# Kernel tuning notes

Measured on AMD Instinct MI355X. Metric: run time of the kernel, lower is better.

Reference implementation:

```python
import jax, jax.numpy as jnp
import numpy as np

B, T, R = 128, 20, 49           # batch, caption length, num regions (7x7)
V, E, H, FD, A = 10000, 512, 512, 512, 256  # vocab, embed, hidden, feature, attn dims


def setup_inputs() -> dict:
    key = jax.random.key(0)
    ks = jax.random.split(key, 16)
    s = 0.02
    return {
        "features": jax.random.normal(ks[0], (B, R, FD), dtype=jnp.float32),
        "captions": jax.random.randint(ks[1], (B, T), 0, V),
        "emb": jax.random.normal(ks[2], (V, E), dtype=jnp.float32) * s,
        "W_h": jax.random.normal(ks[3], (A, H), dtype=jnp.float32) * s,
        "b_h": jnp.zeros((A,), jnp.float32),
        "W_f": jax.random.normal(ks[4], (A, FD), dtype=jnp.float32) * s,
        "b_f": jnp.zeros((A,), jnp.float32),
        "v_w": jax.random.normal(ks[5], (A,), dtype=jnp.float32) * s,
        "v_b": jnp.zeros((), jnp.float32),
        "W_ih": jax.random.normal(ks[6], (4 * H, E + FD), dtype=jnp.float32) * s,
        "W_hh": jax.random.normal(ks[7], (4 * H, H), dtype=jnp.float32) * s,
        "b_ih": jnp.zeros((4 * H,), jnp.float32),
        "b_hh": jnp.zeros((4 * H,), jnp.float32),
        "fc_W": jax.random.normal(ks[8], (V, H), dtype=jnp.float32) * s,
        "fc_b": jnp.zeros((V,), jnp.float32),
    }


def reference(features, captions, emb, W_h, b_h, W_f, b_f, v_w, v_b,
              W_ih, W_hh, b_ih, b_hh, fc_W, fc_b):
    Bn = features.shape[0]
    Hd = W_hh.shape[1]
    # features are constant across timesteps -> project once (same math as per-step W_f(features))
    f_proj = jnp.einsum('brf,af->bra', features, W_f) + b_f  # (B,R,A)
    embeds = emb[captions[:, :-1]]                            # (B,T-1,E)
    xs = jnp.swapaxes(embeds, 0, 1)                           # (T-1,B,E)
    bias = b_ih + b_hh

    def step(carry, x_t):
        hx, cx = carry
        # Bahdanau attention
        h = hx @ W_h.T + b_h                                  # (B,A)
        scores = jnp.tanh(h[:, None, :] + f_proj) @ v_w + v_b  # (B,R)
        alpha = jax.nn.softmax(scores, axis=1)
        context = jnp.einsum('br,brf->bf', alpha, features)   # (B,FD)
        # LSTMCell (PyTorch gate order: i,f,g,o)
        lstm_in = jnp.concatenate([x_t, context], axis=1)     # (B,E+FD)
        gates = lstm_in @ W_ih.T + hx @ W_hh.T + bias         # (B,4H)
        i, f, g, o = jnp.split(gates, 4, axis=1)
        cx = jax.nn.sigmoid(f) * cx + jax.nn.sigmoid(i) * jnp.tanh(g)
        hx = jax.nn.sigmoid(o) * jnp.tanh(cx)
        logit = hx @ fc_W.T + fc_b                            # (B,V)
        return (hx, cx), logit

    init = (jnp.zeros((Bn, Hd), features.dtype), jnp.zeros((Bn, Hd), features.dtype))
    _, logits = jax.lax.scan(step, init, xs)                  # (T-1,B,V)
    return jnp.swapaxes(logits, 0, 1)                         # (B,T-1,V)
```

## Files before the change

### kernel.cpp

```cpp
#include <hip/hip_runtime.h>
#include <hip/hip_bf16.h>
#include <math.h>

#define NB 128
#define NT 20
#define NS 19
#define NR 49
#define NV 10000
#define NE 512
#define NH 512
#define NFD 512
#define NA 256
#define NG 2048
#define NKC 1536

typedef __bf16 bf16_t;
typedef bf16_t bf16x8 __attribute__((ext_vector_type(8)));
typedef float f32x4 __attribute__((ext_vector_type(4)));

__device__ __forceinline__ float sigm(float x) { return 1.f / (1.f + expf(-x)); }

__global__ __launch_bounds__(256) void k_setup(
    const float* __restrict__ W_ih, const float* __restrict__ W_hh,
    const float* __restrict__ b_ih, const float* __restrict__ b_hh,
    const float* __restrict__ W_h, const float* __restrict__ fc_W,
    const float* __restrict__ W_f, const float* __restrict__ features,
    bf16_t* __restrict__ Wcatb, bf16_t* __restrict__ fcWb,
    bf16_t* __restrict__ Wfb, bf16_t* __restrict__ featb,
    bf16_t* __restrict__ W_hb, float* __restrict__ bias,
    float* __restrict__ hx, float* __restrict__ cx)
{
    int idx = blockIdx.x * 256 + threadIdx.x;
    if (idx < NV * NH) fcWb[idx] = (bf16_t)fc_W[idx];
    if (idx < NG * NKC) {
        int n = idx / NKC, k = idx % NKC;
        int h = n >> 2, g = n & 3;
        int orig = g * NH + h;
        Wcatb[idx] = (bf16_t)((k < NE + NFD) ? W_ih[orig * (NE + NFD) + k]
                                             : W_hh[orig * NH + (k - NE - NFD)]);
    }
    if (idx < NB * NR * NFD) featb[idx] = (bf16_t)features[idx];
    if (idx < NA * NFD) Wfb[idx] = (bf16_t)W_f[idx];
    if (idx < NA * NH) W_hb[idx] = (bf16_t)W_h[idx];
    if (idx < NG) {
        int h = idx >> 2, g = idx & 3;
        int orig = g * NH + h;
        bias[idx] = b_ih[orig] + b_hh[orig];
    }
    if (idx < NB * NH) { hx[idx] = 0.f; cx[idx] = 0.f; }
}

__global__ __launch_bounds__(1024) void k_attn(
    const float* __restrict__ hx, const bf16_t* __restrict__ W_hb,
    const float* __restrict__ b_h, const float* __restrict__ fproj,
    const float* __restrict__ v_w, const bf16_t* __restrict__ featb,
    const float* __restrict__ emb, const int* __restrict__ captions,
    bf16_t* __restrict__ lin, int t)
{
    int b = blockIdx.x;
    int tid = threadIdx.x;
    __shared__ float hxs[NH];
    __shared__ float part[4][NA];
    __shared__ float hatt[NA];
    __shared__ float salpha[64];

    if (tid < NH) hxs[tid] = hx[b * NH + tid];
    __syncthreads();

    {
        int a = tid & (NA - 1), q = tid >> 8;
        const bf16x8* wrow = (const bf16x8*)(W_hb + (size_t)a * NH + q * 128);
        const float* hq = hxs + q * 128;
        float p = 0.f;
        #pragma unroll
        for (int c = 0; c < 16; ++c) {
            bf16x8 wv = wrow[c];
            int k = c * 8;
            p += hq[k+0]*(float)wv[0] + hq[k+1]*(float)wv[1]
               + hq[k+2]*(float)wv[2] + hq[k+3]*(float)wv[3]
               + hq[k+4]*(float)wv[4] + hq[k+5]*(float)wv[5]
               + hq[k+6]*(float)wv[6] + hq[k+7]*(float)wv[7];
        }
        part[q][a] = p;
    }
    __syncthreads();
    if (tid < NA)
        hatt[tid] = part[0][tid] + part[1][tid] + part[2][tid] + part[3][tid] + b_h[tid];
    __syncthreads();

    {
        int wv = tid >> 6, lane = tid & 63;
        for (int r = wv; r < NR; r += 16) {
            float s = 0.f;
            const float* fp = fproj + (size_t)(b * NR + r) * NA;
            #pragma unroll
            for (int j = 0; j < 4; ++j) {
                int aa = lane + 64 * j;
                s += tanhf(hatt[aa] + fp[aa]) * v_w[aa];
            }
            #pragma unroll
            for (int off = 32; off; off >>= 1) s += __shfl_xor(s, off);
            if (lane == 0) salpha[r] = s;
        }
    }
    __syncthreads();

    if (tid < 64) {
        float v = (tid < NR) ? salpha[tid] : -INFINITY;
        float m = v;
        #pragma unroll
        for (int off = 32; off; off >>= 1) m = fmaxf(m, __shfl_xor(m, off));
        float e = (tid < NR) ? expf(v - m) : 0.f;
        float ssum = e;
        #pragma unroll
        for (int off = 32; off; off >>= 1) ssum += __shfl_xor(ssum, off);
        if (tid < NR) salpha[tid] = e / ssum;
    }
    __syncthreads();

    if (tid < NH) {
        bf16_t* lrow = lin + (size_t)b * NKC;
        lrow[tid] = (bf16_t)emb[(size_t)captions[b * NT + t] * NE + tid];
        lrow[NE + NFD + tid] = (bf16_t)hxs[tid];
        float c = 0.f;
        #pragma unroll 7
        for (int r = 0; r < NR; ++r)
            c += salpha[r] * (float)featb[(size_t)(b * NR + r) * NFD + tid];
        lrow[NE + tid] = (bf16_t)c;
    }
}

__global__ __launch_bounds__(256) void gemm_bf16_nt(
    const bf16_t* __restrict__ Am, const bf16_t* __restrict__ Bm,
    const float* __restrict__ bias, float* __restrict__ Cm,
    int M, int N, int K, int ldc)
{
    __shared__ uint4 AsU[512];
    __shared__ uint4 BsU[512];
    int tid = threadIdx.x;
    int m0 = blockIdx.x * 64, n0 = blockIdx.y * 64;
    int nk = K >> 6;

    int rowS = tid >> 3, slotS = tid & 7;
    int wr0 = rowS * 8 + (slotS ^ (rowS & 7));
    int rowS2 = rowS + 32;
    int wr1 = rowS2 * 8 + (slotS ^ (rowS2 & 7));

    const uint4* pA = (const uint4*)(Am + (size_t)(m0 + rowS) * K) + slotS;
    size_t aStep = (size_t)4 * K;
    int nrow0 = n0 + rowS, nrow1 = n0 + rowS2;
    bool bv0 = nrow0 < N, bv1 = nrow1 < N;
    const uint4* pB0 = (const uint4*)(Bm + (size_t)nrow0 * K) + slotS;
    const uint4* pB1 = (const uint4*)(Bm + (size_t)nrow1 * K) + slotS;
    uint4 zz = make_uint4(0, 0, 0, 0);

    int w = tid >> 6, lane = tid & 63;
    int wm = w >> 1, wn = w & 1;
    int lr = lane & 15, lg = lane >> 4;
    int ra[2][2], rb[2][2];
    #pragma unroll
    for (int i = 0; i < 2; ++i)
        #pragma unroll
        for (int kk = 0; kk < 2; ++kk) {
            int rA = wm * 32 + i * 16 + lr;
            int rB = wn * 32 + i * 16 + lr;
            int s = kk * 4 + lg;
            ra[i][kk] = rA * 8 + (s ^ (rA & 7));
            rb[i][kk] = rB * 8 + (s ^ (rB & 7));
        }

    f32x4 acc00 = {}, acc01 = {}, acc10 = {}, acc11 = {};
    uint4 a0 = pA[0], a1 = pA[aStep];
    uint4 b0 = bv0 ? pB0[0] : zz;
    uint4 b1 = bv1 ? pB1[0] : zz;
    pA += 8; pB0 += 8; pB1 += 8;

    for (int kt = 0; kt < nk; ++kt) {
        __syncthreads();
        AsU[wr0] = a0; AsU[wr1] = a1;
        BsU[wr0] = b0; BsU[wr1] = b1;
        if (kt + 1 < nk) {
            a0 = pA[0]; a1 = pA[aStep];
            b0 = bv0 ? pB0[0] : zz;
            b1 = bv1 ? pB1[0] : zz;
            pA += 8; pB0 += 8; pB1 += 8;
        }
        __syncthreads();
        const bf16x8* Af = (const bf16x8*)AsU;
        const bf16x8* Bf = (const bf16x8*)BsU;
        #pragma unroll
        for (int kk = 0; kk < 2; ++kk) {
            bf16x8 fa0 = Af[ra[0][kk]], fa1 = Af[ra[1][kk]];
            bf16x8 fb0 = Bf[rb[0][kk]], fb1 = Bf[rb[1][kk]];
            acc00 = __builtin_amdgcn_mfma_f32_16x16x32_bf16(fa0, fb0, acc00, 0, 0, 0);
            acc01 = __builtin_amdgcn_mfma_f32_16x16x32_bf16(fa0, fb1, acc01, 0, 0, 0);
            acc10 = __builtin_amdgcn_mfma_f32_16x16x32_bf16(fa1, fb0, acc10, 0, 0, 0);
            acc11 = __builtin_amdgcn_mfma_f32_16x16x32_bf16(fa1, fb1, acc11, 0, 0, 0);
        }
    }

    f32x4 av[2][2] = {{acc00, acc01}, {acc10, acc11}};
    #pragma unroll
    for (int i = 0; i < 2; ++i) {
        int mbase = m0 + wm * 32 + i * 16 + lg * 4;
        #pragma unroll
        for (int j = 0; j < 2; ++j) {
            int n = n0 + wn * 32 + j * 16 + lr;
            if (n < N) {
                float bz = bias ? bias[n] : 0.f;
                #pragma unroll
                for (int r = 0; r < 4; ++r)
                    Cm[(size_t)(mbase + r) * ldc + n] = av[i][j][r] + bz;
            }
        }
    }
}

__global__ __launch_bounds__(256) void k_step(
    const bf16_t* __restrict__ lin, const bf16_t* __restrict__ Wcatb,
    const float* __restrict__ bias, float* __restrict__ hx,
    float* __restrict__ cx, bf16_t* __restrict__ hxAll, int t)
{
    __shared__ __align__(16) char smem[16640];
    uint4* AsU = (uint4*)smem;
    uint4* BsU = AsU + 512;

    int tid = threadIdx.x;
    int m0 = blockIdx.x * 64, n0 = blockIdx.y * 64;

    int rowS = tid >> 3, slotS = tid & 7;
    int wr0 = rowS * 8 + (slotS ^ (rowS & 7));
    int rowS2 = rowS + 32;
    int wr1 = rowS2 * 8 + (slotS ^ (rowS2 & 7));

    const uint4* pA = (const uint4*)(lin + (size_t)(m0 + rowS) * NKC) + slotS;
    const uint4* pB0 = (const uint4*)(Wcatb + (size_t)(n0 + rowS) * NKC) + slotS;
    const uint4* pB1 = (const uint4*)(Wcatb + (size_t)(n0 + rowS2) * NKC) + slotS;
    size_t aStep = (size_t)4 * NKC;

    int w = tid >> 6, lane = tid & 63;
    int wm = w >> 1, wn = w & 1;
    int lr = lane & 15, lg = lane >> 4;
    int ra[2][2], rb[2][2];
    #pragma unroll
    for (int i = 0; i < 2; ++i)
        #pragma unroll
        for (int kk = 0; kk < 2; ++kk) {
            int rA = wm * 32 + i * 16 + lr;
            int rB = wn * 32 + i * 16 + lr;
            int s = kk * 4 + lg;
            ra[i][kk] = rA * 8 + (s ^ (rA & 7));
            rb[i][kk] = rB * 8 + (s ^ (rB & 7));
        }

    f32x4 acc00 = {}, acc01 = {}, acc10 = {}, acc11 = {};
    uint4 a0 = pA[0], a1 = pA[aStep];
    uint4 b0 = pB0[0], b1 = pB1[0];
    pA += 8; pB0 += 8; pB1 += 8;

    #pragma unroll 1
    for (int kt = 0; kt < NKC / 64; ++kt) {
        __syncthreads();
        AsU[wr0] = a0; AsU[wr1] = a1;
        BsU[wr0] = b0; BsU[wr1] = b1;
        if (kt + 1 < NKC / 64) {
            a0 = pA[0]; a1 = pA[aStep];
            b0 = pB0[0]; b1 = pB1[0];
            pA += 8; pB0 += 8; pB1 += 8;
        }
        __syncthreads();
        const bf16x8* Af = (const bf16x8*)AsU;
        const bf16x8* Bf = (const bf16x8*)BsU;
        #pragma unroll
        for (int kk = 0; kk < 2; ++kk) {
            bf16x8 fa0 = Af[ra[0][kk]], fa1 = Af[ra[1][kk]];
            bf16x8 fb0 = Bf[rb[0][kk]], fb1 = Bf[rb[1][kk]];
            acc00 = __builtin_amdgcn_mfma_f32_16x16x32_bf16(fa0, fb0, acc00, 0, 0, 0);
            acc01 = __builtin_amdgcn_mfma_f32_16x16x32_bf16(fa0, fb1, acc01, 0, 0, 0);
            acc10 = __builtin_amdgcn_mfma_f32_16x16x32_bf16(fa1, fb0, acc10, 0, 0, 0);
            acc11 = __builtin_amdgcn_mfma_f32_16x16x32_bf16(fa1, fb1, acc11, 0, 0, 0);
        }
    }

    __syncthreads();
    float* Ct = (float*)smem;
    f32x4 av[2][2] = {{acc00, acc01}, {acc10, acc11}};
    #pragma unroll
    for (int i = 0; i < 2; ++i)
        #pragma unroll
        for (int j = 0; j < 2; ++j) {
            int mloc = wm * 32 + i * 16 + lg * 4;
            int nloc = wn * 32 + j * 16 + lr;
            #pragma unroll
            for (int r = 0; r < 4; ++r)
                Ct[(mloc + r) * 65 + nloc] = av[i][j][r];
        }
    __syncthreads();

    int hloc = tid & 15;
    int h = (n0 >> 2) + hloc;
    #pragma unroll
    for (int q = 0; q < 4; ++q) {
        int m = (tid >> 4) + q * 16;
        int b = m0 + m;
        const float* crow = Ct + m * 65 + hloc * 4;
        const float* brow = bias + n0 + hloc * 4;
        float gi = crow[0] + brow[0];
        float gf = crow[1] + brow[1];
        float gg = crow[2] + brow[2];
        float go = crow[3] + brow[3];
        size_t idx = (size_t)b * NH + h;
        float c = sigm(gf) * cx[idx] + sigm(gi) * tanhf(gg);
        float hn = sigm(go) * tanhf(c);
        cx[idx] = c;
        hx[idx] = hn;
        hxAll[((size_t)t * NB + b) * NH + h] = (bf16_t)hn;
    }
}

__global__ __launch_bounds__(256) void k_logits(
    const bf16_t* __restrict__ hxAll, const bf16_t* __restrict__ fcWb,
    const float* __restrict__ fc_b, float* __restrict__ out)
{
    __shared__ uint4 AsU[512];
    __shared__ uint4 BsU[512];
    int tid = threadIdx.x;
    int m0 = blockIdx.x * 64, n0 = blockIdx.y * 64;

    int rowS = tid >> 3, slotS = tid & 7;
    int wr0 = rowS * 8 + (slotS ^ (rowS & 7));
    int rowS2 = rowS + 32;
    int wr1 = rowS2 * 8 + (slotS ^ (rowS2 & 7));

    const uint4* pA = (const uint4*)(hxAll + (size_t)(m0 + rowS) * NH) + slotS;
    size_t aStep = (size_t)4 * NH;
    int nrow0 = n0 + rowS, nrow1 = n0 + rowS2;
    bool bv0 = nrow0 < NV, bv1 = nrow1 < NV;
    const uint4* pB0 = (const uint4*)(fcWb + (size_t)nrow0 * NH) + slotS;
    const uint4* pB1 = (const uint4*)(fcWb + (size_t)nrow1 * NH) + slotS;
    uint4 zz = make_uint4(0, 0, 0, 0);

    int w = tid >> 6, lane = tid & 63;
    int wm = w >> 1, wn = w & 1;
    int lr = lane & 15, lg = lane >> 4;
    int ra[2][2], rb[2][2];
    #pragma unroll
    for (int i = 0; i < 2; ++i)
        #pragma unroll
        for (int kk = 0; kk < 2; ++kk) {
            int rA = wm * 32 + i * 16 + lr;
            int rB = wn * 32 + i * 16 + lr;
            int s = kk * 4 + lg;
            ra[i][kk] = rA * 8 + (s ^ (rA & 7));
            rb[i][kk] = rB * 8 + (s ^ (rB & 7));
        }

    f32x4 acc00 = {}, acc01 = {}, acc10 = {}, acc11 = {};
    uint4 a0 = pA[0], a1 = pA[aStep];
    uint4 b0 = bv0 ? pB0[0] : zz;
    uint4 b1 = bv1 ? pB1[0] : zz;
    pA += 8; pB0 += 8; pB1 += 8;

    #pragma unroll 1
    for (int kt = 0; kt < NH / 64; ++kt) {
        __syncthreads();
        AsU[wr0] = a0; AsU[wr1] = a1;
        BsU[wr0] = b0; BsU[wr1] = b1;
        if (kt + 1 < NH / 64) {
            a0 = pA[0]; a1 = pA[aStep];
            b0 = bv0 ? pB0[0] : zz;
            b1 = bv1 ? pB1[0] : zz;
            pA += 8; pB0 += 8; pB1 += 8;
        }
        __syncthreads();
        const bf16x8* Af = (const bf16x8*)AsU;
        const bf16x8* Bf = (const bf16x8*)BsU;
        #pragma unroll
        for (int kk = 0; kk < 2; ++kk) {
            bf16x8 fa0 = Af[ra[0][kk]], fa1 = Af[ra[1][kk]];
            bf16x8 fb0 = Bf[rb[0][kk]], fb1 = Bf[rb[1][kk]];
            acc00 = __builtin_amdgcn_mfma_f32_16x16x32_bf16(fa0, fb0, acc00, 0, 0, 0);
            acc01 = __builtin_amdgcn_mfma_f32_16x16x32_bf16(fa0, fb1, acc01, 0, 0, 0);
            acc10 = __builtin_amdgcn_mfma_f32_16x16x32_bf16(fa1, fb0, acc10, 0, 0, 0);
            acc11 = __builtin_amdgcn_mfma_f32_16x16x32_bf16(fa1, fb1, acc11, 0, 0, 0);
        }
    }

    f32x4 av[2][2] = {{acc00, acc01}, {acc10, acc11}};
    #pragma unroll
    for (int i = 0; i < 2; ++i) {
        int mbase = m0 + wm * 32 + i * 16 + lg * 4;
        #pragma unroll
        for (int j = 0; j < 2; ++j) {
            int n = n0 + wn * 32 + j * 16 + lr;
            if (n < NV) {
                float bz = fc_b[n];
                #pragma unroll
                for (int r = 0; r < 4; ++r) {
                    int m = mbase + r;
                    int b = m & 127, tt = m >> 7;
                    out[((size_t)b * NS + tt) * NV + n] = av[i][j][r] + bz;
                }
            }
        }
    }
}

extern "C" void kernel_launch(void* const* d_in, const int* in_sizes, int n_in,
                              void* d_out, int out_size, void* d_ws, size_t ws_size,
                              hipStream_t stream)
{
    const float* features = (const float*)d_in[0];
    const int*   captions = (const int*)d_in[1];
    const float* emb      = (const float*)d_in[2];
    const float* W_h      = (const float*)d_in[3];
    const float* b_h      = (const float*)d_in[4];
    const float* W_f      = (const float*)d_in[5];
    const float* b_f      = (const float*)d_in[6];
    const float* v_w      = (const float*)d_in[7];
    const float* W_ih     = (const float*)d_in[9];
    const float* W_hh     = (const float*)d_in[10];
    const float* b_ih     = (const float*)d_in[11];
    const float* b_hh     = (const float*)d_in[12];
    const float* fc_W     = (const float*)d_in[13];
    const float* fc_b     = (const float*)d_in[14];
    float* out = (float*)d_out;

    char* base = (char*)d_ws;
    bf16_t* Wcatb = (bf16_t*)base;  base += (size_t)NG * NKC * 2;
    bf16_t* fcWb  = (bf16_t*)base;  base += (size_t)NV * NH * 2;
    bf16_t* Wfb   = (bf16_t*)base;  base += (size_t)NA * NFD * 2;
    bf16_t* featb = (bf16_t*)base;  base += (size_t)NB * NR * NFD * 2;
    bf16_t* lin   = (bf16_t*)base;  base += (size_t)NB * NKC * 2;
    bf16_t* W_hb  = (bf16_t*)base;  base += (size_t)NA * NH * 2;
    bf16_t* hxAll = (bf16_t*)base;  base += (size_t)NS * NB * NH * 2;
    float* bias   = (float*)base;   base += (size_t)NG * 4;
    float* fproj  = (float*)base;   base += (size_t)NB * NR * NA * 4;
    float* hx     = (float*)base;   base += (size_t)NB * NH * 4;
    float* cx     = (float*)base;   base += (size_t)NB * NH * 4;

    k_setup<<<dim3((NV * NH + 255) / 256), 256, 0, stream>>>(
        W_ih, W_hh, b_ih, b_hh, W_h, fc_W, W_f, features,
        Wcatb, fcWb, Wfb, featb, W_hb, bias, hx, cx);

    gemm_bf16_nt<<<dim3(98, 4), 256, 0, stream>>>(
        featb, Wfb, b_f, fproj, NB * NR, NA, NFD, NA);

    for (int t = 0; t < NS; ++t) {
        k_attn<<<dim3(NB), 1024, 0, stream>>>(
            hx, W_hb, b_h, fproj, v_w, featb, emb, captions, lin, t);
        k_step<<<dim3(2, 32), 256, 0, stream>>>(
            lin, Wcatb, bias, hx, cx, hxAll, t);
    }

    k_logits<<<dim3(38, 157), 256, 0, stream>>>(hxAll, fcWb, fc_b, out);
}
```

Baseline: 682.5 us.

## Fuse recurrent attention and LSTM steps into one persistent cooperative kernel

Replaces the 38 per-timestep launches (attention kernel plus LSTM gate GEMM) with a single cooperative persistent kernel of 128 blocks. The blocks synchronise through an atomic-counter grid barrier between the attention phase and the gate GEMM phase. The gate GEMM is retiled to 32x64 tiles so 128 blocks cover it. The logits GEMM also gets a one-dimensional grid with an XCD-aware block swizzle. This removes launch overhead and inter-kernel gaps, at the cost of spin-wait barriers and lower per-step parallelism, since attention now uses 512 threads per batch row.

```diff
diff --git a/kernel.cpp b/kernel.cpp
--- a/kernel.cpp
+++ b/kernel.cpp
@@ -13,12 +13,26 @@
 #define NA 256
 #define NG 2048
 #define NKC 1536
+#define NBLK 128
 
 typedef __bf16 bf16_t;
 typedef bf16_t bf16x8 __attribute__((ext_vector_type(8)));
 typedef float f32x4 __attribute__((ext_vector_type(4)));
 
 __device__ __forceinline__ float sigm(float x) { return 1.f / (1.f + expf(-x)); }
+
+__device__ __forceinline__ void grid_sync(unsigned* cnt, unsigned target)
+{
+    __syncthreads();
+    if (threadIdx.x == 0) {
+        __threadfence();
+        atomicAdd(cnt, 1u);
+        while (__hip_atomic_load(cnt, __ATOMIC_RELAXED, __HIP_MEMORY_SCOPE_AGENT) < target)
+            __builtin_amdgcn_s_sleep(1);
+        __threadfence();
+    }
+    __syncthreads();
+}
 
 __global__ __launch_bounds__(256) void k_setup(
     const float* __restrict__ W_ih, const float* __restrict__ W_hh,
@@ -50,86 +64,6 @@
     if (idx < NB * NH) { hx[idx] = 0.f; cx[idx] = 0.f; }
 }
 
-__global__ __launch_bounds__(1024) void k_attn(
-    const float* __restrict__ hx, const bf16_t* __restrict__ W_hb,
-    const float* __restrict__ b_h, const float* __restrict__ fproj,
-    const float* __restrict__ v_w, const bf16_t* __restrict__ featb,
-    const float* __restrict__ emb, const int* __restrict__ captions,
-    bf16_t* __restrict__ lin, int t)
-{
-    int b = blockIdx.x;
-    int tid = threadIdx.x;
-    __shared__ float hxs[NH];
-    __shared__ float part[4][NA];
-    __shared__ float hatt[NA];
-    __shared__ float salpha[64];
-
-    if (tid < NH) hxs[tid] = hx[b * NH + tid];
-    __syncthreads();
-
-    {
-        int a = tid & (NA - 1), q = tid >> 8;
-        const bf16x8* wrow = (const bf16x8*)(W_hb + (size_t)a * NH + q * 128);
-        const float* hq = hxs + q * 128;
-        float p = 0.f;
-        #pragma unroll
-        for (int c = 0; c < 16; ++c) {
-            bf16x8 wv = wrow[c];
-            int k = c * 8;
-            p += hq[k+0]*(float)wv[0] + hq[k+1]*(float)wv[1]
-               + hq[k+2]*(float)wv[2] + hq[k+3]*(float)wv[3]
-               + hq[k+4]*(float)wv[4] + hq[k+5]*(float)wv[5]
-               + hq[k+6]*(float)wv[6] + hq[k+7]*(float)wv[7];
-        }
-        part[q][a] = p;
-    }
-    __syncthreads();
-    if (tid < NA)
-        hatt[tid] = part[0][tid] + part[1][tid] + part[2][tid] + part[3][tid] + b_h[tid];
-    __syncthreads();
-
-    {
-        int wv = tid >> 6, lane = tid & 63;
-        for (int r = wv; r < NR; r += 16) {
-            float s = 0.f;
-            const float* fp = fproj + (size_t)(b * NR + r) * NA;
-            #pragma unroll
-            for (int j = 0; j < 4; ++j) {
-                int aa = lane + 64 * j;
-                s += tanhf(hatt[aa] + fp[aa]) * v_w[aa];
-            }
-            #pragma unroll
-            for (int off = 32; off; off >>= 1) s += __shfl_xor(s, off);
-            if (lane == 0) salpha[r] = s;
-        }
-    }
-    __syncthreads();
-
-    if (tid < 64) {
-        float v = (tid < NR) ? salpha[tid] : -INFINITY;
-        float m = v;
-        #pragma unroll
-        for (int off = 32; off; off >>= 1) m = fmaxf(m, __shfl_xor(m, off));
-        float e = (tid < NR) ? expf(v - m) : 0.f;
-        float ssum = e;
-        #pragma unroll
-        for (int off = 32; off; off >>= 1) ssum += __shfl_xor(ssum, off);
-        if (tid < NR) salpha[tid] = e / ssum;
-    }
-    __syncthreads();
-
-    if (tid < NH) {
-        bf16_t* lrow = lin + (size_t)b * NKC;
-        lrow[tid] = (bf16_t)emb[(size_t)captions[b * NT + t] * NE + tid];
-        lrow[NE + NFD + tid] = (bf16_t)hxs[tid];
-        float c = 0.f;
-        #pragma unroll 7
-        for (int r = 0; r < NR; ++r)
-            c += salpha[r] * (float)featb[(size_t)(b * NR + r) * NFD + tid];
-        lrow[NE + tid] = (bf16_t)c;
-    }
-}
-
 __global__ __launch_bounds__(256) void gemm_bf16_nt(
     const bf16_t* __restrict__ Am, const bf16_t* __restrict__ Bm,
     const float* __restrict__ bias, float* __restrict__ Cm,
@@ -216,27 +150,194 @@
     }
 }
 
-__global__ __launch_bounds__(256) void k_step(
-    const bf16_t* __restrict__ lin, const bf16_t* __restrict__ Wcatb,
-    const float* __restrict__ bias, float* __restrict__ hx,
-    float* __restrict__ cx, bf16_t* __restrict__ hxAll, int t)
-{
-    __shared__ __align__(16) char smem[16640];
-    uint4* AsU = (uint4*)smem;
-    uint4* BsU = AsU + 512;
+__global__ __launch_bounds__(512) void k_loop(
+    const bf16_t* __restrict__ Wcatb, const bf16_t* __restrict__ W_hb,
+    const float* __restrict__ b_h, const float* __restrict__ fproj,
+    const float* __restrict__ v_w, const bf16_t* __restrict__ featb,
+    const float* __restrict__ emb, const int* __restrict__ captions,
+    const float* __restrict__ bias,
+    bf16_t* __restrict__ lin, float* __restrict__ hx, float* __restrict__ cx,
+    bf16_t* __restrict__ hxAll, unsigned* __restrict__ bar)
+{
+    __shared__ union {
+        struct { float hxs[NH]; float part[2][NA]; float salpha[64]; } att;
+        struct { uint4 AsU[256]; uint4 BsU[512]; } g;
+        float Ct[32 * 65];
+    } sm;
 
     int tid = threadIdx.x;
-    int m0 = blockIdx.x * 64, n0 = blockIdx.y * 64;
+    int bid = blockIdx.x;
+    int lane = tid & 63;
+    unsigned bcount = 0;
+
+    int m0 = (bid & 3) * 32;
+    int n0 = (bid >> 2) * 64;
+    int sRow = tid >> 3, sSlot = tid & 7;
+    int wrS = sRow * 8 + (sSlot ^ (sRow & 7));
+    const uint4* pB_base = (const uint4*)(Wcatb + (size_t)(n0 + sRow) * NKC) + sSlot;
+    const uint4* pA_base = (tid < 256)
+        ? (const uint4*)(lin + (size_t)(m0 + sRow) * NKC) + sSlot : (const uint4*)0;
+
+    int w = tid >> 6;
+    int wm = w & 1, wn = w >> 1;
+    int lr = lane & 15, lg = lane >> 4;
+    int raIdx[2], rbIdx[2];
+    #pragma unroll
+    for (int kk = 0; kk < 2; ++kk) {
+        int rA = wm * 16 + lr;
+        int rB = wn * 16 + lr;
+        int s = kk * 4 + lg;
+        raIdx[kk] = rA * 8 + (s ^ (rA & 7));
+        rbIdx[kk] = rB * 8 + (s ^ (rB & 7));
+    }
+
+    for (int t = 0; t < NS; ++t) {
+        int b = bid;
+        sm.att.hxs[tid] = hx[b * NH + tid];
+        __syncthreads();
+        {
+            int a = tid & 255, q = tid >> 8;
+            const bf16x8* wrow = (const bf16x8*)(W_hb + (size_t)a * NH + q * 256);
+            const float* hq = sm.att.hxs + q * 256;
+            float p = 0.f;
+            #pragma unroll
+            for (int c2 = 0; c2 < 32; ++c2) {
+                bf16x8 wv = wrow[c2];
+                int k = c2 * 8;
+                p += hq[k+0]*(float)wv[0] + hq[k+1]*(float)wv[1]
+                   + hq[k+2]*(float)wv[2] + hq[k+3]*(float)wv[3]
+                   + hq[k+4]*(float)wv[4] + hq[k+5]*(float)wv[5]
+                   + hq[k+6]*(float)wv[6] + hq[k+7]*(float)wv[7];
+            }
+            sm.att.part[q][a] = p;
+        }
+        __syncthreads();
+        {
+            for (int r = w; r < NR; r += 8) {
+                const float* fp = fproj + ((size_t)b * NR + r) * NA;
+                float s = 0.f;
+                #pragma unroll
+                for (int j = 0; j < 4; ++j) {
+                    int aa = lane + 64 * j;
+                    float hv = sm.att.part[0][aa] + sm.att.part[1][aa] + b_h[aa];
+                    s += tanhf(hv + fp[aa]) * v_w[aa];
+                }
+                #pragma unroll
+                for (int off = 32; off; off >>= 1) s += __shfl_xor(s, off);
+                if (lane == 0) sm.att.salpha[r] = s;
+            }
+        }
+        __syncthreads();
+        if (tid < 64) {
+            float v = (tid < NR) ? sm.att.salpha[tid] : -INFINITY;
+            float m = v;
+            #pragma unroll
+            for (int off = 32; off; off >>= 1) m = fmaxf(m, __shfl_xor(m, off));
+            float e = (tid < NR) ? expf(v - m) : 0.f;
+            float ssum = e;
+            #pragma unroll
+            for (int off = 32; off; off >>= 1) ssum += __shfl_xor(ssum, off);
+            if (tid < NR) sm.att.salpha[tid] = e / ssum;
+        }
+        __syncthreads();
+        {
+            bf16_t* lrow = lin + (size_t)b * NKC;
+            int cap = captions[b * NT + t];
+            lrow[tid] = (bf16_t)emb[(size_t)cap * NE + tid];
+            lrow[NE + NFD + tid] = (bf16_t)sm.att.hxs[tid];
+            float c = 0.f;
+            #pragma unroll 7
+            for (int r = 0; r < NR; ++r)
+                c += sm.att.salpha[r] * (float)featb[((size_t)b * NR + r) * NFD + tid];
+            lrow[NE + tid] = (bf16_t)c;
+        }
+        grid_sync(bar, (++bcount) * NBLK);
+
+        {
+            const uint4* pA = pA_base;
+            const uint4* pB = pB_base;
+            f32x4 acc = {};
+            uint4 aR = {}, bR;
+            bR = pB[0]; pB += 8;
+            if (tid < 256) { aR = pA[0]; pA += 8; }
+            #pragma unroll 1
+            for (int kt = 0; kt < NKC / 64; ++kt) {
+                __syncthreads();
+                sm.g.BsU[wrS] = bR;
+                if (tid < 256) sm.g.AsU[wrS] = aR;
+                if (kt + 1 < NKC / 64) {
+                    bR = pB[0]; pB += 8;
+                    if (tid < 256) { aR = pA[0]; pA += 8; }
+                }
+                __syncthreads();
+                const bf16x8* Af = (const bf16x8*)sm.g.AsU;
+                const bf16x8* Bf = (const bf16x8*)sm.g.BsU;
+                #pragma unroll
+                for (int kk = 0; kk < 2; ++kk) {
+                    bf16x8 fa = Af[raIdx[kk]];
+                    bf16x8 fb = Bf[rbIdx[kk]];
+                    acc = __builtin_amdgcn_mfma_f32_16x16x32_bf16(fa, fb, acc, 0, 0, 0);
+                }
+            }
+            __syncthreads();
+            {
+                int crow = wm * 16 + lg * 4;
+                int ccol = wn * 16 + lr;
+                #pragma unroll
+                for (int r = 0; r < 4; ++r)
+                    sm.Ct[(crow + r) * 65 + ccol] = acc[r];
+            }
+            __syncthreads();
+            {
+                int hloc = tid & 15, m = tid >> 4;
+                int bb = m0 + m;
+                int h = (n0 >> 2) + hloc;
+                const float* crow = sm.Ct + m * 65 + hloc * 4;
+                const float* brow = bias + n0 + hloc * 4;
+                float gi = crow[0] + brow[0];
+                float gf = crow[1] + brow[1];
+                float gg = crow[2] + brow[2];
+                float go = crow[3] + brow[3];
+                size_t idx = (size_t)bb * NH + h;
+                float c = sigm(gf) * cx[idx] + sigm(gi) * tanhf(gg);
+                float hn = sigm(go) * tanhf(c);
+                cx[idx] = c;
+                hx[idx] = hn;
+                hxAll[((size_t)t * NB + bb) * NH + h] = (bf16_t)hn;
+            }
+        }
+        grid_sync(bar, (++bcount) * NBLK);
+    }
+}
+
+__global__ __launch_bounds__(256) void k_logits(
+    const bf16_t* __restrict__ hxAll, const bf16_t* __restrict__ fcWb,
+    const float* __restrict__ fc_b, float* __restrict__ out)
+{
+    const int MT = 38, NWG = 38 * 157;
+    int bid0 = blockIdx.x;
+    int q = NWG >> 3, r = NWG & 7;
+    int xcd = bid0 & 7, loc = bid0 >> 3;
+    int swz = (xcd < r ? xcd * (q + 1) : r * (q + 1) + (xcd - r) * q) + loc;
+    int m0 = (swz % MT) * 64;
+    int n0 = (swz / MT) * 64;
+
+    __shared__ uint4 AsU[512];
+    __shared__ uint4 BsU[512];
+    int tid = threadIdx.x;
 
     int rowS = tid >> 3, slotS = tid & 7;
     int wr0 = rowS * 8 + (slotS ^ (rowS & 7));
     int rowS2 = rowS + 32;
     int wr1 = rowS2 * 8 + (slotS ^ (rowS2 & 7));
 
-    const uint4* pA = (const uint4*)(lin + (size_t)(m0 + rowS) * NKC) + slotS;
-    const uint4* pB0 = (const uint4*)(Wcatb + (size_t)(n0 + rowS) * NKC) + slotS;
-    const uint4* pB1 = (const uint4*)(Wcatb + (size_t)(n0 + rowS2) * NKC) + slotS;
-    size_t aStep = (size_t)4 * NKC;
+    const uint4* pA = (const uint4*)(hxAll + (size_t)(m0 + rowS) * NH) + slotS;
+    size_t aStep = (size_t)4 * NH;
+    int nrow0 = n0 + rowS, nrow1 = n0 + rowS2;
+    bool bv0 = nrow0 < NV, bv1 = nrow1 < NV;
+    const uint4* pB0 = (const uint4*)(fcWb + (size_t)nrow0 * NH) + slotS;
+    const uint4* pB1 = (const uint4*)(fcWb + (size_t)nrow1 * NH) + slotS;
+    uint4 zz = make_uint4(0, 0, 0, 0);
 
     int w = tid >> 6, lane = tid & 63;
     int wm = w >> 1, wn = w & 1;
@@ -255,17 +356,19 @@
 
     f32x4 acc00 = {}, acc01 = {}, acc10 = {}, acc11 = {};
     uint4 a0 = pA[0], a1 = pA[aStep];
-    uint4 b0 = pB0[0], b1 = pB1[0];
+    uint4 b0 = bv0 ? pB0[0] : zz;
+    uint4 b1 = bv1 ? pB1[0] : zz;
     pA += 8; pB0 += 8; pB1 += 8;
 
     #pragma unroll 1
-    for (int kt = 0; kt < NKC / 64; ++kt) {
+    for (int kt = 0; kt < NH / 64; ++kt) {
         __syncthreads();
         AsU[wr0] = a0; AsU[wr1] = a1;
         BsU[wr0] = b0; BsU[wr1] = b1;
-        if (kt + 1 < NKC / 64) {
+        if (kt + 1 < NH / 64) {
             a0 = pA[0]; a1 = pA[aStep];
-            b0 = pB0[0]; b1 = pB1[0];
+            b0 = bv0 ? pB0[0] : zz;
+            b1 = bv1 ? pB1[0] : zz;
             pA += 8; pB0 += 8; pB1 += 8;
         }
         __syncthreads();
@@ -282,110 +385,6 @@
         }
     }
 
-    __syncthreads();
-    float* Ct = (float*)smem;
-    f32x4 av[2][2] = {{acc00, acc01}, {acc10, acc11}};
-    #pragma unroll
-    for (int i = 0; i < 2; ++i)
-        #pragma unroll
-        for (int j = 0; j < 2; ++j) {
-            int mloc = wm * 32 + i * 16 + lg * 4;
-            int nloc = wn * 32 + j * 16 + lr;
-            #pragma unroll
-            for (int r = 0; r < 4; ++r)
-                Ct[(mloc + r) * 65 + nloc] = av[i][j][r];
-        }
-    __syncthreads();
-
-    int hloc = tid & 15;
-    int h = (n0 >> 2) + hloc;
-    #pragma unroll
-    for (int q = 0; q < 4; ++q) {
-        int m = (tid >> 4) + q * 16;
-        int b = m0 + m;
-        const float* crow = Ct + m * 65 + hloc * 4;
-        const float* brow = bias + n0 + hloc * 4;
-        float gi = crow[0] + brow[0];
-        float gf = crow[1] + brow[1];
-        float gg = crow[2] + brow[2];
-        float go = crow[3] + brow[3];
-        size_t idx = (size_t)b * NH + h;
-        float c = sigm(gf) * cx[idx] + sigm(gi) * tanhf(gg);
-        float hn = sigm(go) * tanhf(c);
-        cx[idx] = c;
-        hx[idx] = hn;
-        hxAll[((size_t)t * NB + b) * NH + h] = (bf16_t)hn;
-    }
-}
-
-__global__ __launch_bounds__(256) void k_logits(
-    const bf16_t* __restrict__ hxAll, const bf16_t* __restrict__ fcWb,
-    const float* __restrict__ fc_b, float* __restrict__ out)
-{
-    __shared__ uint4 AsU[512];
-    __shared__ uint4 BsU[512];
-    int tid = threadIdx.x;
-    int m0 = blockIdx.x * 64, n0 = blockIdx.y * 64;
-
-    int rowS = tid >> 3, slotS = tid & 7;
-    int wr0 = rowS * 8 + (slotS ^ (rowS & 7));
-    int rowS2 = rowS + 32;
-    int wr1 = rowS2 * 8 + (slotS ^ (rowS2 & 7));
-
-    const uint4* pA = (const uint4*)(hxAll + (size_t)(m0 + rowS) * NH) + slotS;
-    size_t aStep = (size_t)4 * NH;
-    int nrow0 = n0 + rowS, nrow1 = n0 + rowS2;
-    bool bv0 = nrow0 < NV, bv1 = nrow1 < NV;
-    const uint4* pB0 = (const uint4*)(fcWb + (size_t)nrow0 * NH) + slotS;
-    const uint4* pB1 = (const uint4*)(fcWb + (size_t)nrow1 * NH) + slotS;
-    uint4 zz = make_uint4(0, 0, 0, 0);
-
-    int w = tid >> 6, lane = tid & 63;
-    int wm = w >> 1, wn = w & 1;
-    int lr = lane & 15, lg = lane >> 4;
-    int ra[2][2], rb[2][2];
-    #pragma unroll
-    for (int i = 0; i < 2; ++i)
-        #pragma unroll
-        for (int kk = 0; kk < 2; ++kk) {
-            int rA = wm * 32 + i * 16 + lr;
-            int rB = wn * 32 + i * 16 + lr;
-            int s = kk * 4 + lg;
-            ra[i][kk] = rA * 8 + (s ^ (rA & 7));
-            rb[i][kk] = rB * 8 + (s ^ (rB & 7));
-        }
-
-    f32x4 acc00 = {}, acc01 = {}, acc10 = {}, acc11 = {};
-    uint4 a0 = pA[0], a1 = pA[aStep];
-    uint4 b0 = bv0 ? pB0[0] : zz;
-    uint4 b1 = bv1 ? pB1[0] : zz;
-    pA += 8; pB0 += 8; pB1 += 8;
-
-    #pragma unroll 1
-    for (int kt = 0; kt < NH / 64; ++kt) {
-        __syncthreads();
-        AsU[wr0] = a0; AsU[wr1] = a1;
-        BsU[wr0] = b0; BsU[wr1] = b1;
-        if (kt + 1 < NH / 64) {
-            a0 = pA[0]; a1 = pA[aStep];
-            b0 = bv0 ? pB0[0] : zz;
-            b1 = bv1 ? pB1[0] : zz;
-            pA += 8; pB0 += 8; pB1 += 8;
-        }
-        __syncthreads();
-        const bf16x8* Af = (const bf16x8*)AsU;
-        const bf16x8* Bf = (const bf16x8*)BsU;
-        #pragma unroll
-        for (int kk = 0; kk < 2; ++kk) {
-            bf16x8 fa0 = Af[ra[0][kk]], fa1 = Af[ra[1][kk]];
-            bf16x8 fb0 = Bf[rb[0][kk]], fb1 = Bf[rb[1][kk]];
-            acc00 = __builtin_amdgcn_mfma_f32_16x16x32_bf16(fa0, fb0, acc00, 0, 0, 0);
-            acc01 = __builtin_amdgcn_mfma_f32_16x16x32_bf16(fa0, fb1, acc01, 0, 0, 0);
-            acc10 = __builtin_amdgcn_mfma_f32_16x16x32_bf16(fa1, fb0, acc10, 0, 0, 0);
-            acc11 = __builtin_amdgcn_mfma_f32_16x16x32_bf16(fa1, fb1, acc11, 0, 0, 0);
-        }
-    }
-
     f32x4 av[2][2] = {{acc00, acc01}, {acc10, acc11}};
     #pragma unroll
     for (int i = 0; i < 2; ++i) {
@@ -398,8 +397,8 @@
                 #pragma unroll
                 for (int r = 0; r < 4; ++r) {
                     int m = mbase + r;
-                    int b = m & 127, tt = m >> 7;
-                    out[((size_t)b * NS + tt) * NV + n] = av[i][j][r] + bz;
+                    int bb = m & 127, tt = m >> 7;
+                    out[((size_t)bb * NS + tt) * NV + n] = av[i][j][r] + bz;
                 }
             }
         }
@@ -427,6 +426,7 @@
     float* out = (float*)d_out;
 
     char* base = (char*)d_ws;
+    unsigned* bar = (unsigned*)base; base += 256;
     bf16_t* Wcatb = (bf16_t*)base;  base += (size_t)NG * NKC * 2;
     bf16_t* fcWb  = (bf16_t*)base;  base += (size_t)NV * NH * 2;
     bf16_t* Wfb   = (bf16_t*)base;  base += (size_t)NA * NFD * 2;
@@ -439,6 +439,8 @@
     float* hx     = (float*)base;   base += (size_t)NB * NH * 4;
     float* cx     = (float*)base;   base += (size_t)NB * NH * 4;
 
+    hipMemsetAsync(bar, 0, sizeof(unsigned), stream);
+
     k_setup<<<dim3((NV * NH + 255) / 256), 256, 0, stream>>>(
         W_ih, W_hh, b_ih, b_hh, W_h, fc_W, W_f, features,
         Wcatb, fcWb, Wfb, featb, W_hb, bias, hx, cx);
@@ -446,12 +448,13 @@
     gemm_bf16_nt<<<dim3(98, 4), 256, 0, stream>>>(
         featb, Wfb, b_f, fproj, NB * NR, NA, NFD, NA);
 
-    for (int t = 0; t < NS; ++t) {
-        k_attn<<<dim3(NB), 1024, 0, stream>>>(
-            hx, W_hb, b_h, fproj, v_w, featb, emb, captions, lin, t);
-        k_step<<<dim3(2, 32), 256, 0, stream>>>(
-            lin, Wcatb, bias, hx, cx, hxAll, t);
-    }
-
-    k_logits<<<dim3(38, 157), 256, 0, stream>>>(hxAll, fcWb, fc_b, out);
-}
+    void* kargs[] = {
+        (void*)&Wcatb, (void*)&W_hb, (void*)&b_h, (void*)&fproj,
+        (void*)&v_w, (void*)&featb, (void*)&emb, (void*)&captions,
+        (void*)&bias, (void*)&lin, (void*)&hx, (void*)&cx,
+        (void*)&hxAll, (void*)&bar };
+    hipLaunchCooperativeKernel((const void*)k_loop, dim3(NBLK), dim3(512),
+                               kargs, 0, stream);
+
+    k_logits<<<dim3(38 * 157), 256, 0, stream>>>(hxAll, fcWb, fc_b, out);
+}
```

Result: slower. 1.475 ms (+116.2%).
